# Performance work log

Measured on AMD Instinct MI355X. Metric: run time of the kernel, lower is better.

The kernel has to match this reference:

```python
import jax, jax.numpy as jnp
import numpy as np
import math

D_MODEL = 1024
NHEAD = 16
FACTOR = 1
B, L = 2, 4096


def setup_inputs() -> dict:
    key = jax.random.key(0)
    ks = jax.random.split(key, 12)
    s = 0.02
    inp = {
        "query": jax.random.normal(ks[0], (B, L, D_MODEL), dtype=jnp.float32),
        "key": jax.random.normal(ks[1], (B, L, D_MODEL), dtype=jnp.float32),
        "value": jax.random.normal(ks[2], (B, L, D_MODEL), dtype=jnp.float32),
        "Wq": jax.random.normal(ks[3], (D_MODEL, D_MODEL), dtype=jnp.float32) * s,
        "bq": jnp.zeros((D_MODEL,), dtype=jnp.float32),
        "Wk": jax.random.normal(ks[4], (D_MODEL, D_MODEL), dtype=jnp.float32) * s,
        "bk": jnp.zeros((D_MODEL,), dtype=jnp.float32),
        "Wv": jax.random.normal(ks[5], (D_MODEL, D_MODEL), dtype=jnp.float32) * s,
        "bv": jnp.zeros((D_MODEL,), dtype=jnp.float32),
        "Wo": jax.random.normal(ks[6], (D_MODEL, D_MODEL), dtype=jnp.float32) * s,
        "bo": jnp.zeros((D_MODEL,), dtype=jnp.float32),
    }
    return inp


def _autocorr_forward(query, key, value, Wq, bq, Wk, bk, Wv, bv, Wo, bo):
    Bq, Lq, d = query.shape
    Lk = key.shape[1]
    H = NHEAD
    Dk = d // H

    # projections, split heads -> (B, H, L, Dk)
    Q = (query @ Wq + bq).reshape(Bq, Lq, H, Dk).transpose(0, 2, 1, 3)
    K = (key @ Wk + bk).reshape(Bq, Lk, H, Dk).transpose(0, 2, 1, 3)
    V = (value @ Wv + bv).reshape(Bq, Lk, H, Dk).transpose(0, 2, 1, 3)

    # align K/V sequence length to L_q (truncate or zero-pad)
    if Lk > Lq:
        K = K[:, :, :Lq, :]
        V = V[:, :, :Lq, :]
    elif Lq > Lk:
        pad = [(0, 0), (0, 0), (0, Lq - Lk), (0, 0)]
        K = jnp.pad(K, pad)
        V = jnp.pad(V, pad)
    Lloc = Lq

    # FFT-based circular autocorrelation along the sequence axis
    Qf = jnp.fft.rfft(Q, axis=2)
    Kf = jnp.fft.rfft(K, axis=2)
    corr = jnp.fft.irfft(Qf * jnp.conj(Kf), n=Lloc, axis=2)  # (B,H,L,Dk)
    corr_mean = corr.mean(axis=-1)  # (B,H,L)

    top_k = min(max(1, int(FACTOR * math.log(Lloc + 1))), Lloc)
    w, idx = jax.lax.top_k(corr_mean, top_k)  # (B,H,k)
    w = jax.nn.softmax(w, axis=-1)

    # circular gather of V at each delay, weighted combine over top-k delays
    ar = jnp.arange(Lloc)
    shifted = (ar[None, None, None, :] + idx[..., None]) % Lloc  # (B,H,k,L)
    rolled = jnp.take_along_axis(
        V[:, :, None, :, :], shifted[..., None], axis=3
    )  # (B,H,k,L,Dk)
    out = jnp.einsum("bhk,bhkld->bhld", w, rolled)  # (B,H,L,Dk)

    out = out.transpose(0, 2, 1, 3).reshape(Bq, Lq, d)
    return out @ Wo + bo  # dropout is identity in eval mode


def reference(query, key, value, Wq, bq, Wk, bk, Wv, bv, Wo, bo):
    return _autocorr_forward(query, key, value, Wq, bq, Wk, bk, Wv, bv, Wo, bo)
```

## Files before the change

### kernel.cpp

```cpp
#include <hip/hip_runtime.h>
#include <hip/hip_bf16.h>

#define LL 4096
#define NH 16
#define DM 1024
#define DK 64
#define MTOT 8192
#define PI_F 3.14159265358979323846f

typedef short short8 __attribute__((ext_vector_type(8)));
typedef float f32x4 __attribute__((ext_vector_type(4)));

typedef __attribute__((address_space(1))) const unsigned char g_u8;
typedef __attribute__((address_space(3))) unsigned char l_u8;

__device__ __forceinline__ void gload16(const void* g, void* l){
  __builtin_amdgcn_global_load_lds((g_u8*)g, (l_u8*)l, 16, 0, 0);
}

__device__ __forceinline__ unsigned short f2bf(float x){
  union { float f; unsigned int u; } v; v.f = x;
  unsigned int r = v.u + 0x7FFFu + ((v.u >> 16) & 1u);
  return (unsigned short)(r >> 16);
}
__device__ __forceinline__ float bf2f(unsigned short u){
  union { unsigned int u; float f; } v; v.u = ((unsigned int)u) << 16; return v.f;
}

__global__ void k_conv_x(const float* __restrict__ in, unsigned short* __restrict__ out, int n4){
  int i = blockIdx.x*256 + threadIdx.x;
  if (i >= n4) return;
  float4 v = ((const float4*)in)[i];
  ushort4 o; o.x=f2bf(v.x); o.y=f2bf(v.y); o.z=f2bf(v.z); o.w=f2bf(v.w);
  ((ushort4*)out)[i] = o;
}

__global__ void k_conv_x_split2(const float* __restrict__ q, const float* __restrict__ k,
                                unsigned short* __restrict__ hi, unsigned short* __restrict__ lo, int n4){
  int i = blockIdx.x*256 + threadIdx.x;
  float4 v = (i < n4) ? ((const float4*)q)[i] : ((const float4*)k)[i - n4];
  ushort4 oh, ol;
  oh.x=f2bf(v.x); ol.x=f2bf(v.x - bf2f(oh.x));
  oh.y=f2bf(v.y); ol.y=f2bf(v.y - bf2f(oh.y));
  oh.z=f2bf(v.z); ol.z=f2bf(v.z - bf2f(oh.z));
  oh.w=f2bf(v.w); ol.w=f2bf(v.w - bf2f(oh.w));
  ((ushort4*)hi)[i] = oh;
  ((ushort4*)lo)[i] = ol;
}

__global__ void k_conv_wt(const float* __restrict__ W0, const float* __restrict__ W1,
                          const float* __restrict__ W2, const float* __restrict__ W3,
                          unsigned short* __restrict__ hi_base, unsigned short* __restrict__ lo_base){
  const float* W = (blockIdx.z==0)?W0:(blockIdx.z==1)?W1:(blockIdx.z==2)?W2:W3;
  unsigned short* oh = hi_base + (size_t)blockIdx.z*DM*DM;
  unsigned short* ol = (blockIdx.z<2) ? (lo_base + (size_t)blockIdx.z*DM*DM) : nullptr;
  __shared__ unsigned short th[64][65];
  __shared__ unsigned short tl[64][65];
  int n0 = blockIdx.x*64, k0 = blockIdx.y*64;
  for (int i=0;i<16;i++){
    int g = i*256 + threadIdx.x;
    int kr = g>>6, nc = g&63;
    float x = W[(size_t)(k0+kr)*DM + n0+nc];
    unsigned short h = f2bf(x);
    th[kr][nc] = h;
    tl[kr][nc] = f2bf(x - bf2f(h));
  }
  __syncthreads();
  for (int i=0;i<16;i++){
    int g = i*256 + threadIdx.x;
    int nr = g>>6, kc = g&63;
    oh[(size_t)(n0+nr)*DM + k0+kc] = th[kc][nr];
    if (ol) ol[(size_t)(n0+nr)*DM + k0+kc] = tl[kc][nr];
  }
}

template<int MODE>
__global__ __launch_bounds__(256) void k_gemm_plain(
    const short* __restrict__ A, const short* __restrict__ Bt,
    const float* __restrict__ bias, float* __restrict__ Cf, unsigned short* __restrict__ Cb)
{
  __shared__ short As[128][64];
  __shared__ short Bs[128][64];
  const int m0 = blockIdx.x*128, n0 = blockIdx.y*128;
  const int tid = threadIdx.x;
  const int wave = tid>>6, lane = tid&63;
  const int wm = (wave>>1)*64, wn = (wave&1)*64;
  const int li = lane&15, lk4 = lane>>4;
  const int srow = lane>>3, scol = (lane&7)*8;
  f32x4 acc[4][4] = {};
  for (int kt=0; kt<16; ++kt){
    #pragma unroll
    for (int c=0;c<4;c++){
      int q = wave*4+c;
      int row = q*8 + srow;
      gload16(&A [(size_t)(m0+row)*DM + kt*64 + scol], &As[q*8][0]);
      gload16(&Bt[(size_t)(n0+row)*DM + kt*64 + scol], &Bs[q*8][0]);
    }
    __syncthreads();
    #pragma unroll
    for (int kk=0; kk<64; kk+=32){
      short8 af[4], bfv[4];
      #pragma unroll
      for (int mi=0;mi<4;mi++) af[mi] = *(const short8*)&As[wm+mi*16+li][kk+lk4*8];
      #pragma unroll
      for (int ni=0;ni<4;ni++) bfv[ni] = *(const short8*)&Bs[wn+ni*16+li][kk+lk4*8];
      #pragma unroll
      for (int mi=0;mi<4;mi++)
        #pragma unroll
        for (int ni=0;ni<4;ni++)
          acc[mi][ni] = __builtin_amdgcn_mfma_f32_16x16x32_bf16(af[mi], bfv[ni], acc[mi][ni], 0,0,0);
    }
    __syncthreads();
  }
  #pragma unroll
  for (int mi=0;mi<4;mi++){
    #pragma unroll
    for (int ni=0;ni<4;ni++){
      const int col = n0 + wn + ni*16 + li;
      const float bv = bias[col];
      const int mbase = m0 + wm + mi*16 + lk4*4;
      #pragma unroll
      for (int r=0;r<4;r++){
        const int row = mbase + r;
        float v = acc[mi][ni][r] + bv;
        if (MODE==2){
          Cf[(size_t)row*DM + col] = v;
        } else {
          int b = row>>12, l = row&(LL-1), h = col>>6, d = col&63;
          Cb[(((size_t)(b*NH+h))*LL + l)*DK + d] = f2bf(v);
        }
      }
    }
  }
}

__global__ __launch_bounds__(512, 2) void k_gemm_split256(
    const short* __restrict__ Ahi, const short* __restrict__ Alo,
    const short* __restrict__ Whi, const short* __restrict__ Wlo,
    const float* __restrict__ bias_q, const float* __restrict__ bias_k,
    float* __restrict__ OutQ, float* __restrict__ OutK, int nq)
{
  __shared__ short AsH[2][256][32];
  __shared__ short AsL[2][256][32];
  __shared__ short BsH[2][256][32];
  __shared__ short BsL[2][256][32];

  const int side = (blockIdx.x >= nq) ? 1 : 0;
  const int m0 = blockIdx.x*256, n0 = blockIdx.y*256;
  const short* Bhi = Whi + (size_t)side*DM*DM;
  const short* Blo = Wlo + (size_t)side*DM*DM;
  const float* bias = side ? bias_k : bias_q;
  float* Ct = side ? OutK : OutQ;
  const int ml0 = m0 - side*(nq*256);

  const int tid = threadIdx.x;
  const int wave = tid>>6, lane = tid&63;
  const int wm = (wave>>2)*128;
  const int wn = (wave&3)*64;
  const int li = lane&15, lk4 = lane>>4;
  const int srow = lane>>2;
  const int scol = (lane&3)*8;

  f32x4 acc[8][4] = {};

  auto STAGE = [&](int kt, int bufi){
    const int kof = kt*32 + scol;
    #pragma unroll
    for (int s=0;s<2;s++){
      const int r = s*128 + wave*16;
      const int gr = r + srow;
      gload16(&Ahi[(size_t)(m0+gr)*DM + kof], &AsH[bufi][r][0]);
      gload16(&Alo[(size_t)(m0+gr)*DM + kof], &AsL[bufi][r][0]);
      gload16(&Bhi[(size_t)(n0+gr)*DM + kof], &BsH[bufi][r][0]);
      gload16(&Blo[(size_t)(n0+gr)*DM + kof], &BsL[bufi][r][0]);
    }
  };

  STAGE(0, 0);
  __syncthreads();

  for (int kt=0; kt<32; ++kt){
    const int cur = kt&1;
    if (kt < 31) STAGE(kt+1, cur^1);

    short8 bhf[4], blf[4];
    #pragma unroll
    for (int ni=0;ni<4;ni++){
      bhf[ni] = *(const short8*)&BsH[cur][wn+ni*16+li][lk4*8];
      blf[ni] = *(const short8*)&BsL[cur][wn+ni*16+li][lk4*8];
    }
    #pragma unroll
    for (int p=0;p<4;p++){
      short8 ah0 = *(const short8*)&AsH[cur][wm+(2*p  )*16+li][lk4*8];
      short8 al0 = *(const short8*)&AsL[cur][wm+(2*p  )*16+li][lk4*8];
      short8 ah1 = *(const short8*)&AsH[cur][wm+(2*p+1)*16+li][lk4*8];
      short8 al1 = *(const short8*)&AsL[cur][wm+(2*p+1)*16+li][lk4*8];
      __builtin_amdgcn_s_setprio(1);
      #pragma unroll
      for (int ni=0;ni<4;ni++){
        f32x4 a0 = acc[2*p][ni];
        a0 = __builtin_amdgcn_mfma_f32_16x16x32_bf16(ah0, bhf[ni], a0, 0,0,0);
        a0 = __builtin_amdgcn_mfma_f32_16x16x32_bf16(ah0, blf[ni], a0, 0,0,0);
        a0 = __builtin_amdgcn_mfma_f32_16x16x32_bf16(al0, bhf[ni], a0, 0,0,0);
        acc[2*p][ni] = a0;
        f32x4 a1 = acc[2*p+1][ni];
        a1 = __builtin_amdgcn_mfma_f32_16x16x32_bf16(ah1, bhf[ni], a1, 0,0,0);
        a1 = __builtin_amdgcn_mfma_f32_16x16x32_bf16(ah1, blf[ni], a1, 0,0,0);
        a1 = __builtin_amdgcn_mfma_f32_16x16x32_bf16(al1, bhf[ni], a1, 0,0,0);
        acc[2*p+1][ni] = a1;
      }
      __builtin_amdgcn_s_setprio(0);
    }
    __syncthreads();
  }

  #pragma unroll
  for (int mi=0;mi<8;mi++){
    #pragma unroll
    for (int ni=0;ni<4;ni++){
      const int col = n0 + wn + ni*16 + li;
      const float bv = bias[col];
      const int mbase = ml0 + wm + mi*16 + lk4*4;
      const int b = mbase>>12, l0 = mbase&(LL-1);
      const int h = col>>6, d = col&63;
      float4 o;
      o.x = acc[mi][ni][0]+bv; o.y = acc[mi][ni][1]+bv;
      o.z = acc[mi][ni][2]+bv; o.w = acc[mi][ni][3]+bv;
      *(float4*)&Ct[(((size_t)(b*NH+h))*DK + d)*LL + l0] = o;
    }
  }
}

__device__ __forceinline__ float2 cmul(float2 a, float2 b){
  return make_float2(a.x*b.x - a.y*b.y, a.x*b.y + a.y*b.x);
}
__device__ __forceinline__ int swz(int i){ return i ^ ((i>>4)&15); }

__device__ __forceinline__ float2 ctw(float2 v, int k, float sgn){
  float c, s;
  switch(k){
    case 0: return v;
    case 1: c= 0.92387953251f; s= 0.38268343236f; break;
    case 2: c= 0.70710678119f; s= 0.70710678119f; break;
    case 3: c= 0.38268343236f; s= 0.92387953251f; break;
    case 4: c= 0.f;            s= 1.f;            break;
    case 6: c=-0.70710678119f; s= 0.70710678119f; break;
    default:c=-0.92387953251f; s=-0.38268343236f; break;
  }
  s *= sgn;
  return make_float2(v.x*c - v.y*s, v.x*s + v.y*c);
}

template<int SGN>
__device__ __forceinline__ void dft16(float2 x[16]){
  const float sg = (float)SGN;
  #pragma unroll
  for (int m1=0;m1<4;m1++){
    float2 a=x[m1], b=x[m1+4], c=x[m1+8], d=x[m1+12];
    float acx=a.x+c.x, acy=a.y+c.y, sx=a.x-c.x, sy=a.y-c.y;
    float bdx=b.x+d.x, bdy=b.y+d.y, tx=b.x-d.x, ty=b.y-d.y;
    float ix=-sg*ty, iy=sg*tx;
    x[m1]    = make_float2(acx+bdx, acy+bdy);
    x[m1+4]  = make_float2(sx+ix,  sy+iy);
    x[m1+8]  = make_float2(acx-bdx, acy-bdy);
    x[m1+12] = make_float2(sx-ix,  sy-iy);
  }
  float2 y[16];
  #pragma unroll
  for (int p1=0;p1<4;p1++){
    float2 a = x[4*p1+0];
    float2 b = ctw(x[4*p1+1], p1,   sg);
    float2 c = ctw(x[4*p1+2], 2*p1, sg);
    float2 d = ctw(x[4*p1+3], 3*p1, sg);
    float acx=a.x+c.x, acy=a.y+c.y, sx=a.x-c.x, sy=a.y-c.y;
    float bdx=b.x+d.x, bdy=b.y+d.y, tx=b.x-d.x, ty=b.y-d.y;
    float ix=-sg*ty, iy=sg*tx;
    y[p1]    = make_float2(acx+bdx, acy+bdy);
    y[p1+4]  = make_float2(sx+ix,  sy+iy);
    y[p1+8]  = make_float2(acx-bdx, acy-bdy);
    y[p1+12] = make_float2(sx-ix,  sy-iy);
  }
  #pragma unroll
  for (int i=0;i<16;i++) x[i]=y[i];
}

template<int SGN>
__device__ __forceinline__ void twiddle_apply(float2 x[16], int j, float invden){
  float th = (float)SGN * 6.28318530717958647f * (float)j * invden;
  float s, c; __sincosf(th, &s, &c);
  float2 w1 = make_float2(c, s);
  float2 w2 = cmul(w1,w1), w3 = cmul(w2,w1), w4 = cmul(w2,w2);
  float2 w8 = cmul(w4,w4), w12 = cmul(w8,w4);
  float2 wl[4] = {make_float2(1.f,0.f), w1, w2, w3};
  float2 wh[4] = {make_float2(1.f,0.f), w4, w8, w12};
  #pragma unroll
  for (int m=1;m<16;m++){
    float2 tw = cmul(wh[m>>2], wl[m&3]);
    x[m] = cmul(x[m], tw);
  }
}

template<int SGN>
__device__ __forceinline__ void fft_stages(float2* lds, float2 x[16], int t){
  dft16<SGN>(x);
  #pragma unroll
  for (int p=0;p<16;p++) lds[swz(t*16+p)] = x[p];
  __syncthreads();
  #pragma unroll
  for (int m=0;m<16;m++) x[m] = lds[swz(t + 256*m)];
  __syncthreads();
  twiddle_apply<SGN>(x, t&15, 1.0f/256.0f);
  dft16<SGN>(x);
  {
    int base = (t>>4)*256 + (t&15);
    #pragma unroll
    for (int p=0;p<16;p++) lds[swz(base + 16*p)] = x[p];
  }
  __syncthreads();
  #pragma unroll
  for (int m=0;m<16;m++) x[m] = lds[swz(t + 256*m)];
  __syncthreads();
  twiddle_apply<SGN>(x, t, 1.0f/4096.0f);
  dft16<SGN>(x);
  #pragma unroll
  for (int p=0;p<16;p++) lds[swz(t + 256*p)] = x[p];
  __syncthreads();
}

__global__ __launch_bounds__(256) void k_fft_fwd(const float* __restrict__ Qt, const float* __restrict__ Kt,
                                                 float* __restrict__ Spart){
  __shared__ float2 lds[4096];
  const int bh = blockIdx.x >> 4, g = blockIdx.x & 15;
  const int t = threadIdx.x;
  float2 pacc[16];
  #pragma unroll
  for (int i=0;i<16;i++) pacc[i]=make_float2(0.f,0.f);
  for (int dd=0; dd<4; ++dd){
    const size_t base = ((size_t)bh*DK + g*4 + dd)*LL;
    float2 x[16];
    #pragma unroll
    for (int m=0;m<16;m++){
      int n = t + 256*m;
      x[m] = make_float2(Qt[base+n], Kt[base+n]);
    }
    fft_stages<-1>(lds, x, t);
    #pragma unroll
    for (int i=0;i<16;i++){
      int f = t + 256*i;
      float2 A = lds[swz(f)];
      float2 Bv = lds[swz((LL-f)&(LL-1))];
      float qr = 0.5f*(A.x+Bv.x), qi = 0.5f*(A.y-Bv.y);
      float kr = 0.5f*(A.y+Bv.y), ki = -0.5f*(A.x-Bv.x);
      pacc[i].x += qr*kr + qi*ki;
      pacc[i].y += qi*kr - qr*ki;
    }
    __syncthreads();
  }
  float2* Sp = (float2*)Spart + (size_t)blockIdx.x*LL;
  #pragma unroll
  for (int i=0;i<16;i++) Sp[t + 256*i] = pacc[i];
}

__global__ __launch_bounds__(256) void k_ifft_topk(const float* __restrict__ Spart,
                                                   float* __restrict__ w8, int* __restrict__ idx8){
  __shared__ float2 lds[4096];
  __shared__ float c[4096];
  __shared__ float rv[256];
  __shared__ int   ri[256];
  __shared__ float topv[8];
  __shared__ int   topi[8];
  const int bh = blockIdx.x, t = threadIdx.x;
  float2 x[16];
  #pragma unroll
  for (int m=0;m<16;m++){
    float2 acc = make_float2(0.f,0.f);
    int n = t + 256*m;
    for (int g2=0; g2<16; ++g2){
      float2 v = ((const float2*)Spart)[((size_t)bh*16+g2)*LL + n];
      acc.x += v.x; acc.y += v.y;
    }
    x[m] = acc;
  }
  fft_stages<1>(lds, x, t);
  const float scale = 1.0f/((float)LL * (float)DK);
  #pragma unroll
  for (int m=0;m<16;m++){ int f=t+256*m; c[f] = lds[swz(f)].x * scale; }
  __syncthreads();
  for (int kk=0; kk<8; kk++){
    float bv = -3.4e38f; int bi = 0;
    #pragma unroll
    for (int i=0;i<16;i++){
      int f = t + 256*i;
      float v = c[f];
      if (v > bv || (v == bv && f < bi)) { bv = v; bi = f; }
    }
    rv[t]=bv; ri[t]=bi;
    __syncthreads();
    for (int off=128; off>0; off>>=1){
      if (t < off){
        float ov = rv[t+off]; int oi = ri[t+off];
        if (ov > rv[t] || (ov == rv[t] && oi < ri[t])) { rv[t]=ov; ri[t]=oi; }
      }
      __syncthreads();
    }
    if (t==0){ topv[kk]=rv[0]; topi[kk]=ri[0]; c[ri[0]] = -3.0e38f; }
    __syncthreads();
  }
  if (t==0){
    float m = topv[0];
    float e[8], sum=0.f;
    for (int k=0;k<8;k++){ e[k]=__expf(topv[k]-m); sum+=e[k]; }
    for (int k=0;k<8;k++){ w8[bh*8+k]=e[k]/sum; idx8[bh*8+k]=topi[k]; }
  }
}

__global__ __launch_bounds__(256) void k_gather(const unsigned short* __restrict__ Vh,
                                                const float* __restrict__ w8, const int* __restrict__ idx8,
                                                unsigned short* __restrict__ Ob){
  const int blk = blockIdx.x;
  const int bh = blk >> 6;
  const int l0 = (blk & 63) * 64;
  const int b = bh >> 4, h = bh & 15;
  float w[8]; int ix[8];
  #pragma unroll
  for (int k=0;k<8;k++){ w[k]=w8[bh*8+k]; ix[k]=idx8[bh*8+k]; }
  const int tid = threadIdx.x;
  for (int it=0; it<16; ++it){
    int e = it*256 + tid;
    int lo = e >> 6, d = e & 63;
    int l = l0 + lo;
    float acc = 0.f;
    #pragma unroll
    for (int k=0;k<8;k++){
      int sl = (l + ix[k]) & (LL-1);
      acc += w[k] * bf2f(Vh[((size_t)bh*LL + sl)*DK + d]);
    }
    Ob[((size_t)(b*LL + l))*DM + h*DK + d] = f2bf(acc);
  }
}

extern "C" void kernel_launch(void* const* d_in, const int* in_sizes, int n_in,
                              void* d_out, int out_size, void* d_ws, size_t ws_size,
                              hipStream_t stream) {
  const float* query = (const float*)d_in[0];
  const float* key   = (const float*)d_in[1];
  const float* value = (const float*)d_in[2];
  const float* Wq = (const float*)d_in[3];
  const float* bq = (const float*)d_in[4];
  const float* Wk = (const float*)d_in[5];
  const float* bk = (const float*)d_in[6];
  const float* Wv = (const float*)d_in[7];
  const float* bv = (const float*)d_in[8];
  const float* Wo = (const float*)d_in[9];
  const float* bo = (const float*)d_in[10];
  float* out = (float*)d_out;

  char* ws = (char*)d_ws;
  const int n4 = MTOT*DM/4;
  const size_t MB16 = (size_t)MTOT*DM*2;

  size_t off = 0;
  auto take = [&](size_t b)->char*{ char* p = ws + off; off += (b + 255) & ~(size_t)255; return p; };

  const size_t merged_bytes = 2*(2*MB16) + (size_t)4*DM*DM*2 + (size_t)2*DM*DM*2
                            + 2*((size_t)2*NH*DK*LL*4) + 16384;

  if (ws_size >= merged_bytes) {
    short* Xs_hi = (short*)take(2*MB16);
    short* Xs_lo = (short*)take(2*MB16);
    short* Wth = (short*)take((size_t)4*DM*DM*2);
    short* Wtl = (short*)take((size_t)2*DM*DM*2);
    float* Qt  = (float*)take((size_t)2*NH*DK*LL*4);
    float* Kt  = (float*)take((size_t)2*NH*DK*LL*4);
    float* w8  = (float*)take(32*8*4);
    int*  idx8 = (int*)take(32*8*4);
    float* Spart = (float*)Xs_hi;
    unsigned short* Ob = (unsigned short*)((char*)Xs_hi + MB16);
    unsigned short* Xv = (unsigned short*)Xs_lo;
    unsigned short* Vh = (unsigned short*)((char*)Xs_lo + MB16);

    k_conv_wt<<<dim3(16,16,4),256,0,stream>>>(Wq,Wk,Wv,Wo,(unsigned short*)Wth,(unsigned short*)Wtl);
    k_conv_x_split2<<<2*n4/256,256,0,stream>>>(query,key,(unsigned short*)Xs_hi,(unsigned short*)Xs_lo,n4);
    k_gemm_split256<<<dim3(64,4),512,0,stream>>>(Xs_hi, Xs_lo, Wth, Wtl, bq, bk, Qt, Kt, 32);
    k_conv_x<<<n4/256,256,0,stream>>>(value, Xv, n4);
    k_gemm_plain<1><<<dim3(64,8),256,0,stream>>>((const short*)Xv, Wth + (size_t)2*DM*DM, bv, nullptr, Vh);
    k_fft_fwd<<<512,256,0,stream>>>(Qt, Kt, Spart);
    k_ifft_topk<<<32,256,0,stream>>>(Spart, w8, idx8);
    k_gather<<<2048,256,0,stream>>>(Vh, w8, idx8, Ob);
    k_gemm_plain<2><<<dim3(64,8),256,0,stream>>>((const short*)Ob, Wth + (size_t)3*DM*DM, bo, out, nullptr);
  } else {
    short* Xhi = (short*)take(MB16);
    short* Xlo = (short*)take(MB16);
    short* Wth = (short*)take((size_t)4*DM*DM*2);
    short* Wtl = (short*)take((size_t)2*DM*DM*2);
    float* Qt  = (float*)take((size_t)2*NH*DK*LL*4);
    float* Kt  = (float*)take((size_t)2*NH*DK*LL*4);
    unsigned short* Vh = (unsigned short*)take((size_t)2*NH*LL*DK*2);
    float* w8  = (float*)take(32*8*4);
    int*  idx8 = (int*)take(32*8*4);
    float* Spart = (float*)Xlo;

    k_conv_wt<<<dim3(16,16,4),256,0,stream>>>(Wq,Wk,Wv,Wo,(unsigned short*)Wth,(unsigned short*)Wtl);

    k_conv_x_split2<<<n4/256,256,0,stream>>>(query,query,(unsigned short*)Xhi,(unsigned short*)Xlo,n4);
    k_gemm_split256<<<dim3(32,4),512,0,stream>>>(Xhi, Xlo, Wth, Wtl, bq, bq, Qt, Qt, 32);

    k_conv_x_split2<<<n4/256,256,0,stream>>>(key,key,(unsigned short*)Xhi,(unsigned short*)Xlo,n4);
    k_gemm_split256<<<dim3(32,4),512,0,stream>>>(Xhi, Xlo, Wth + (size_t)DM*DM, Wtl + (size_t)DM*DM,
                                                 bk, bk, Kt, Kt, 32);

    k_conv_x<<<n4/256,256,0,stream>>>(value,(unsigned short*)Xhi,n4);
    k_gemm_plain<1><<<dim3(64,8),256,0,stream>>>(Xhi, Wth + (size_t)2*DM*DM, bv, nullptr, Vh);

    k_fft_fwd<<<512,256,0,stream>>>(Qt, Kt, Spart);
    k_ifft_topk<<<32,256,0,stream>>>(Spart, w8, idx8);
    k_gather<<<2048,256,0,stream>>>(Vh, w8, idx8, (unsigned short*)Xhi);

    k_gemm_plain<2><<<dim3(64,8),256,0,stream>>>(Xhi, Wth + (size_t)3*DM*DM, bo, out, nullptr);
  }
}
```

Before: 268.2 us.

## Swizzle LDS tiles in GEMMs and split prefetch with manual vmcnt waits

Applies an XOR swizzle to the LDS column layout in both the plain bf16 GEMM and the split hi/lo projection GEMM, so the short8 fragment reads avoid bank conflicts. In the split GEMM, the next tile's global-to-LDS load is split into two halves, the second issued midway through the MFMA loop. The generic syncthreads is replaced by explicit s_waitcnt vmcnt plus s_barrier, letting loads overlap compute. This adds risk: the hand-counted vmcnt values must match the issued async LDS loads, and the swizzle indices must match exactly between writes and reads.

```diff
diff --git a/kernel.cpp b/kernel.cpp
--- a/kernel.cpp
+++ b/kernel.cpp
@@ -86,7 +86,8 @@
   const int wave = tid>>6, lane = tid&63;
   const int wm = (wave>>1)*64, wn = (wave&1)*64;
   const int li = lane&15, lk4 = lane>>4;
-  const int srow = lane>>3, scol = (lane&7)*8;
+  const int srow = lane>>3;
+  const int scol = (((lane&7) ^ srow))*8;
   f32x4 acc[4][4] = {};
   for (int kt=0; kt<16; ++kt){
     #pragma unroll
@@ -101,9 +102,11 @@
     for (int kk=0; kk<64; kk+=32){
       short8 af[4], bfv[4];
       #pragma unroll
-      for (int mi=0;mi<4;mi++) af[mi] = *(const short8*)&As[wm+mi*16+li][kk+lk4*8];
+      for (int mi=0;mi<4;mi++)
+        af[mi] = *(const short8*)&As[wm+mi*16+li][((( (kk>>3)+lk4 ) ^ (li&7)))*8];
       #pragma unroll
-      for (int ni=0;ni<4;ni++) bfv[ni] = *(const short8*)&Bs[wn+ni*16+li][kk+lk4*8];
+      for (int ni=0;ni<4;ni++)
+        bfv[ni] = *(const short8*)&Bs[wn+ni*16+li][((( (kk>>3)+lk4 ) ^ (li&7)))*8];
       #pragma unroll
       for (int mi=0;mi<4;mi++)
         #pragma unroll
@@ -158,43 +161,51 @@
   const int wm = (wave>>2)*128;
   const int wn = (wave&3)*64;
   const int li = lane&15, lk4 = lane>>4;
-  const int srow = lane>>2;
-  const int scol = (lane&3)*8;
+
+  const int sr = lane>>2, sc4 = lane&3;
+  const int scol = ((sc4 ^ (sr&3) ^ ((sr>>2)&3)))*8;
+  const int rbyte = ((lk4 ^ (li&3) ^ (li>>2)))*8;
 
   f32x4 acc[8][4] = {};
 
-  auto STAGE = [&](int kt, int bufi){
+  auto STAGE_HALF = [&](int kt, int bufi, int h){
+    const int r0 = h*128 + wave*16;
+    const int gr = r0 + sr;
     const int kof = kt*32 + scol;
-    #pragma unroll
-    for (int s=0;s<2;s++){
-      const int r = s*128 + wave*16;
-      const int gr = r + srow;
-      gload16(&Ahi[(size_t)(m0+gr)*DM + kof], &AsH[bufi][r][0]);
-      gload16(&Alo[(size_t)(m0+gr)*DM + kof], &AsL[bufi][r][0]);
-      gload16(&Bhi[(size_t)(n0+gr)*DM + kof], &BsH[bufi][r][0]);
-      gload16(&Blo[(size_t)(n0+gr)*DM + kof], &BsL[bufi][r][0]);
-    }
+    gload16(&Ahi[(size_t)(m0+gr)*DM + kof], &AsH[bufi][r0][0]);
+    gload16(&Alo[(size_t)(m0+gr)*DM + kof], &AsL[bufi][r0][0]);
+    gload16(&Bhi[(size_t)(n0+gr)*DM + kof], &BsH[bufi][r0][0]);
+    gload16(&Blo[(size_t)(n0+gr)*DM + kof], &BsL[bufi][r0][0]);
   };
 
-  STAGE(0, 0);
-  __syncthreads();
+  STAGE_HALF(0, 0, 0);
+  STAGE_HALF(0, 0, 1);
 
   for (int kt=0; kt<32; ++kt){
     const int cur = kt&1;
-    if (kt < 31) STAGE(kt+1, cur^1);
+    if (kt < 31){
+      STAGE_HALF(kt+1, cur^1, 0);
+      asm volatile("s_waitcnt vmcnt(4)" ::: "memory");
+    } else {
+      asm volatile("s_waitcnt vmcnt(0)" ::: "memory");
+    }
+    asm volatile("" ::: "memory");
+    __builtin_amdgcn_s_barrier();
+    asm volatile("" ::: "memory");
 
     short8 bhf[4], blf[4];
     #pragma unroll
     for (int ni=0;ni<4;ni++){
-      bhf[ni] = *(const short8*)&BsH[cur][wn+ni*16+li][lk4*8];
-      blf[ni] = *(const short8*)&BsL[cur][wn+ni*16+li][lk4*8];
+      bhf[ni] = *(const short8*)&BsH[cur][wn+ni*16+li][rbyte];
+      blf[ni] = *(const short8*)&BsL[cur][wn+ni*16+li][rbyte];
     }
     #pragma unroll
     for (int p=0;p<4;p++){
-      short8 ah0 = *(const short8*)&AsH[cur][wm+(2*p  )*16+li][lk4*8];
-      short8 al0 = *(const short8*)&AsL[cur][wm+(2*p  )*16+li][lk4*8];
-      short8 ah1 = *(const short8*)&AsH[cur][wm+(2*p+1)*16+li][lk4*8];
-      short8 al1 = *(const short8*)&AsL[cur][wm+(2*p+1)*16+li][lk4*8];
+      if (p==2 && kt<31) STAGE_HALF(kt+1, cur^1, 1);
+      short8 ah0 = *(const short8*)&AsH[cur][wm+(2*p  )*16+li][rbyte];
+      short8 al0 = *(const short8*)&AsL[cur][wm+(2*p  )*16+li][rbyte];
+      short8 ah1 = *(const short8*)&AsH[cur][wm+(2*p+1)*16+li][rbyte];
+      short8 al1 = *(const short8*)&AsL[cur][wm+(2*p+1)*16+li][rbyte];
       __builtin_amdgcn_s_setprio(1);
       #pragma unroll
       for (int ni=0;ni<4;ni++){
@@ -211,7 +222,9 @@
       }
       __builtin_amdgcn_s_setprio(0);
     }
-    __syncthreads();
+    asm volatile("" ::: "memory");
+    __builtin_amdgcn_s_barrier();
+    asm volatile("" ::: "memory");
   }
 
   #pragma unroll
```

Result: faster. 250.8 us (-6.5%).
